# Optimization experiments

Measured on AMD Instinct MI355X. Metric: run time of the kernel, lower is better.

Reference implementation:

```python
import jax, jax.numpy as jnp
import numpy as np

NEG_SLOPE = 0.2  # PyG GATConv default negative_slope


def setup_inputs() -> dict:
    key = jax.random.key(0)
    k1, k2, k3, k4, k5, k6 = jax.random.split(key, 6)
    N, E, DIN, DOUT = 100000, 1600000, 128, 64
    x = jax.random.normal(k1, (N, DIN), dtype=jnp.float32)
    edge_index = jax.random.randint(k2, (2, E), 0, N, dtype=jnp.int64)
    # learned params (glorot-like scale)
    W = jax.random.normal(k3, (DIN, DOUT), dtype=jnp.float32) * (1.0 / np.sqrt(DIN))
    att_src = jax.random.normal(k4, (DOUT,), dtype=jnp.float32) * (1.0 / np.sqrt(DOUT))
    att_dst = jax.random.normal(k5, (DOUT,), dtype=jnp.float32) * (1.0 / np.sqrt(DOUT))
    bias = jnp.zeros((DOUT,), dtype=jnp.float32)
    return {"x": x, "edge_index": edge_index, "W": W,
            "att_src": att_src, "att_dst": att_dst, "bias": bias}


def reference(x, edge_index, W, att_src, att_dst, bias):
    N = x.shape[0]
    # add self loops (PyG default add_self_loops=True)
    loop = jnp.arange(N, dtype=edge_index.dtype)
    src = jnp.concatenate([edge_index[0], loop])  # message sources (x_j)
    dst = jnp.concatenate([edge_index[1], loop])  # aggregation targets (x_i)

    h = x @ W                         # [N, C] linear transform (heads=1)
    a_src = h @ att_src               # [N] per-node source score
    a_dst = h @ att_dst               # [N] per-node target score

    # per-edge raw attention: LeakyReLU(alpha_j + alpha_i)
    e = jax.nn.leaky_relu(a_src[src] + a_dst[dst], NEG_SLOPE)  # [Etot]

    # segment softmax over edges grouped by destination node
    e_max = jax.ops.segment_max(e, dst, num_segments=N)        # every node has self loop
    e_exp = jnp.exp(e - e_max[dst])
    e_sum = jax.ops.segment_sum(e_exp, dst, num_segments=N)
    alpha = e_exp / (e_sum[dst] + 1e-16)                       # [Etot]

    # weighted scatter-add aggregation
    out = jax.ops.segment_sum(h[src] * alpha[:, None], dst, num_segments=N)
    return out + bias
```

## Files before the change

### kernel.cpp

```cpp
#include <hip/hip_runtime.h>
#include <cstddef>

#define DIN 128
#define DOUT 64
#define BKT_SHIFT 7
#define BKT_NODES 128
#define CAP 2680
#define CAPP 2816
#define MAXB 800
#define EPB 8192
#define TW 784

#define QDEC (0.25f / 32767.f)
#define QENC (32767.f / 0.25f)

typedef __attribute__((ext_vector_type(8))) short bf16x8;
typedef __attribute__((ext_vector_type(4))) float f32x4;

__device__ __forceinline__ float leakyrelu(float v) { return v > 0.f ? v : 0.2f * v; }

__device__ __forceinline__ unsigned cvtpk(float lo, float hi) {
    unsigned r;
    asm volatile("v_cvt_pk_bf16_f32 %0, %1, %2" : "=v"(r) : "v"(lo), "v"(hi));
    return r;
}
__device__ __forceinline__ bf16x8 cvt8(f32x4 lo, f32x4 hi) {
    union { bf16x8 v; unsigned u[4]; } cv;
    cv.u[0] = cvtpk(lo[0], lo[1]);
    cv.u[1] = cvtpk(lo[2], lo[3]);
    cv.u[2] = cvtpk(hi[0], hi[1]);
    cv.u[3] = cvtpk(hi[2], hi[3]);
    return cv.v;
}

template<int T>
__device__ __forceinline__ int block_incl_scan(int v, int tid, volatile int* wscr) {
    int s = v;
    #pragma unroll
    for (int d = 1; d < 64; d <<= 1) {
        int t = __shfl_up(s, d);
        if ((tid & 63) >= d) s += t;
    }
    if ((tid & 63) == 63) wscr[tid >> 6] = s;
    __syncthreads();
    constexpr int NW = T / 64;
    if (tid < NW) {
        int w = wscr[tid];
        int sw = w;
        #pragma unroll
        for (int d = 1; d < NW; d <<= 1) {
            int t = __shfl_up(sw, d);
            if (tid >= d) sw += t;
        }
        wscr[tid] = sw - w;
    }
    __syncthreads();
    return s + wscr[tid >> 6];
}

__global__ __launch_bounds__(1024) void k_front(
    const float* __restrict__ x, const float* __restrict__ W,
    const float* __restrict__ att_src, const float* __restrict__ att_dst,
    signed char* __restrict__ h8, float2* __restrict__ sa2, float* __restrict__ adst,
    const int* __restrict__ src, const int* __restrict__ dst,
    unsigned int* __restrict__ sorted, int* __restrict__ table,
    int N, int E, int NB, int NBT)
{
    __shared__ unsigned int sbufL[EPB];
    __shared__ int hist[MAXB];
    __shared__ int offA[MAXB + 1];
    __shared__ int wscr[16];
    const int tid = threadIdx.x;

    if (blockIdx.x < NBT) {
        unsigned short* wlds = (unsigned short*)sbufL;
        {
            const int col = tid & 63;
            const int kg  = tid >> 6;
            float v[8];
            #pragma unroll
            for (int i = 0; i < 8; ++i) v[i] = W[(size_t)(kg * 8 + i) * DOUT + col];
            unsigned p0 = cvtpk(v[0], v[1]);
            unsigned p1 = cvtpk(v[2], v[3]);
            unsigned p2 = cvtpk(v[4], v[5]);
            unsigned p3 = cvtpk(v[6], v[7]);
            const int kbyte = (kg * 16) ^ ((col & 15) << 4);
            *reinterpret_cast<uint4*>((char*)wlds + col * 256 + kbyte) =
                make_uint4(p0, p1, p2, p3);
        }
        __syncthreads();

        const int lane = tid & 63, g = lane >> 4, c15 = lane & 15;
        const int n0w = blockIdx.x * 512 + (tid >> 6) * 32;
        if (n0w >= N) return;

        bf16x8 afrag[2][4];
        #pragma unroll
        for (int u = 0; u < 2; ++u) {
            const int arow = min(n0w + u * 16 + c15, N - 1);
            const float* xr = x + (size_t)arow * DIN + g * 8;
            #pragma unroll
            for (int kb = 0; kb < 4; ++kb) {
                f32x4 lo = *reinterpret_cast<const f32x4*>(xr + kb * 32);
                f32x4 hi = *reinterpret_cast<const f32x4*>(xr + kb * 32 + 4);
                afrag[u][kb] = cvt8(lo, hi);
            }
        }

        f32x4 acc[2][4];
        #pragma unroll
        for (int nt = 0; nt < 4; ++nt) {
            f32x4 a0 = {0.f, 0.f, 0.f, 0.f};
            f32x4 a1 = {0.f, 0.f, 0.f, 0.f};
            const int col = nt * 16 + c15;
            #pragma unroll
            for (int kb = 0; kb < 4; ++kb) {
                const int kbyte = (kb * 64 + g * 16) ^ (c15 << 4);
                bf16x8 bfr = *reinterpret_cast<const bf16x8*>(
                    (const char*)wlds + col * 256 + kbyte);
                a0 = __builtin_amdgcn_mfma_f32_16x16x32_bf16(afrag[0][kb], bfr, a0, 0, 0, 0);
                a1 = __builtin_amdgcn_mfma_f32_16x16x32_bf16(afrag[1][kb], bfr, a1, 0, 0, 0);
            }
            acc[0][nt] = a0;
            acc[1][nt] = a1;
        }

        #pragma unroll
        for (int u = 0; u < 2; ++u) {
            float mr[4];
            #pragma unroll
            for (int r = 0; r < 4; ++r) {
                float m = fabsf(acc[u][0][r]);
                #pragma unroll
                for (int nt = 1; nt < 4; ++nt) m = fmaxf(m, fabsf(acc[u][nt][r]));
                mr[r] = m;
            }
            #pragma unroll
            for (int mask = 1; mask < 16; mask <<= 1)
                #pragma unroll
                for (int r = 0; r < 4; ++r) mr[r] = fmaxf(mr[r], __shfl_xor(mr[r], mask));

            float inv[4];
            #pragma unroll
            for (int r = 0; r < 4; ++r) inv[r] = 127.f / fmaxf(mr[r], 1e-20f);

            #pragma unroll
            for (int nt = 0; nt < 4; ++nt)
                #pragma unroll
                for (int r = 0; r < 4; ++r) {
                    int row = n0w + u * 16 + g * 4 + r;
                    if (row < N) {
                        int qi = __float2int_rn(acc[u][nt][r] * inv[r]);
                        qi = max(-127, min(127, qi));
                        h8[(size_t)row * DOUT + nt * 16 + c15] = (signed char)qi;
                    }
                }

            float ps[4] = {0.f, 0.f, 0.f, 0.f}, pd[4] = {0.f, 0.f, 0.f, 0.f};
            #pragma unroll
            for (int nt = 0; nt < 4; ++nt) {
                float as = att_src[nt * 16 + c15];
                float ad = att_dst[nt * 16 + c15];
                #pragma unroll
                for (int r = 0; r < 4; ++r) {
                    ps[r] = fmaf(acc[u][nt][r], as, ps[r]);
                    pd[r] = fmaf(acc[u][nt][r], ad, pd[r]);
                }
            }
            #pragma unroll
            for (int mask = 1; mask < 16; mask <<= 1)
                #pragma unroll
                for (int r = 0; r < 4; ++r) {
                    ps[r] += __shfl_xor(ps[r], mask);
                    pd[r] += __shfl_xor(pd[r], mask);
                }
            #pragma unroll
            for (int r = 0; r < 4; ++r) {
                int row = n0w + u * 16 + g * 4 + r;
                if (c15 == r && row < N) {
                    sa2[row] = make_float2(ps[r], fmaxf(mr[r], 1e-20f) * (1.f / 127.f));
                    adst[row] = pd[r];
                }
            }
        }
        return;
    }

    const int c = blockIdx.x - NBT;
    const int e0 = c * EPB;
    const int cnt = min(EPB, E - e0);

    for (int i = tid; i < NB; i += 1024) hist[i] = 0;
    __syncthreads();

    unsigned pv[8]; int bv[8], rv[8];
    #pragma unroll
    for (int k = 0; k < 8; ++k) {
        int e = e0 + k * 1024 + tid;
        if (e < E) {
            int d = dst[e];
            pv[k] = (unsigned)src[e] | ((unsigned)(d & (BKT_NODES - 1)) << 17);
            bv[k] = d >> BKT_SHIFT;
            rv[k] = atomicAdd(&hist[bv[k]], 1);
        } else bv[k] = -1;
    }
    __syncthreads();

    {
        int v = (tid < NB) ? hist[tid] : 0;
        int incl = block_incl_scan<1024>(v, tid, wscr);
        if (tid < NB) offA[tid + 1] = incl;
        if (tid == 0) offA[0] = 0;
    }
    __syncthreads();

    for (int i = tid; i <= NB; i += 1024) table[(size_t)c * TW + i] = offA[i];

    #pragma unroll
    for (int k = 0; k < 8; ++k)
        if (bv[k] >= 0) sbufL[offA[bv[k]] + rv[k]] = pv[k];
    __syncthreads();

    for (int i = tid; i < cnt; i += 1024)
        sorted[(size_t)c * EPB + i] = sbufL[i];
}

__global__ __launch_bounds__(512) void k_csr(
    const unsigned int* __restrict__ sorted, const int* __restrict__ table,
    const float2* __restrict__ sa2, const float* __restrict__ adst,
    unsigned int* __restrict__ cpk, int2* __restrict__ nspan,
    int N, int NC)
{
    __shared__ unsigned int el[CAP];
    __shared__ float eal[CAP];
    __shared__ unsigned char rnk[CAP];
    __shared__ int cpre[513];
    __shared__ int cs0[512];
    __shared__ int hist[BKT_NODES], offs[BKT_NODES + 1];
    __shared__ float ssumL[BKT_NODES], selfC[BKT_NODES], adL[BKT_NODES];
    __shared__ int wscr[8];

    const int tid = threadIdx.x;
    const int b = blockIdx.x;
    const int n0 = b << BKT_SHIFT;
    const int nn = min(BKT_NODES, N - n0);

    int len = 0;
    if (tid < NC) {
        int s0 = table[(size_t)tid * TW + b];
        len = table[(size_t)tid * TW + b + 1] - s0;
        cs0[tid] = s0;
    }
    {
        int incl = block_incl_scan<512>((tid < NC) ? len : 0, tid, wscr);
        if (tid < NC) cpre[tid + 1] = incl;
        if (tid == 0) cpre[0] = 0;
    }
    if (tid < BKT_NODES) hist[tid] = 0;
    if (tid < nn) {
        int n = n0 + tid;
        float ad = adst[n];
        adL[tid] = ad;
        float2 v = sa2[n];
        float selfA = __expf(leakyrelu(v.x + ad));
        ssumL[tid] = selfA;
        selfC[tid] = selfA * v.y;
    }
    __syncthreads();
    int cnt = cpre[NC]; if (cnt > CAP) cnt = CAP;

    for (int i = tid; i < cnt; i += 512) {
        int lo = 0, hi = NC;
        while (hi - lo > 1) {
            int mid = (lo + hi) >> 1;
            if (cpre[mid] <= i) lo = mid; else hi = mid;
        }
        el[i] = sorted[(size_t)lo * EPB + cs0[lo] + (i - cpre[lo])];
    }
    __syncthreads();

    for (int i = tid; i < cnt; i += 512) {
        unsigned int e = el[i];
        int ln = e >> 17;
        float2 vs = sa2[e & 0x1FFFF];
        float a = __expf(leakyrelu(vs.x + adL[ln]));
        eal[i] = a * vs.y;
        rnk[i] = (unsigned char)atomicAdd(&hist[ln], 1);
        atomicAdd(&ssumL[ln], a);
    }
    __syncthreads();
    if (tid < nn) ssumL[tid] = 1.f / (ssumL[tid] + 1e-16f);

    {
        int v = (tid < BKT_NODES) ? hist[tid] + 1 : 0;
        int incl = block_incl_scan<512>(v, tid, wscr);
        if (tid < BKT_NODES) offs[tid + 1] = incl;
        if (tid == 0) offs[0] = 0;
    }
    __syncthreads();

    const size_t gbase = (size_t)b * CAPP;
    for (int i = tid; i < cnt; i += 512) {
        unsigned int e = el[i];
        int ln = e >> 17;
        unsigned int s = e & 0x1FFFF;
        int p = offs[ln] + (int)rnk[i];
        float cq = eal[i] * ssumL[ln];
        unsigned q = (unsigned)fminf(cq * QENC + 0.5f, 32767.f);
        cpk[gbase + p] = s | (q << 17);
    }
    __syncthreads();

    if (tid < nn) {
        int n = n0 + tid;
        int pend = offs[tid + 1];
        float cq = selfC[tid] * ssumL[tid];
        unsigned q = (unsigned)fminf(cq * QENC + 0.5f, 32767.f);
        cpk[gbase + pend - 1] = (unsigned)n | (q << 17);
        nspan[n] = make_int2((int)gbase + offs[tid], (int)gbase + pend);
    }
}

__global__ __launch_bounds__(256) void k_agg(
    const int2* __restrict__ nspan, const unsigned int* __restrict__ cpk,
    const signed char* __restrict__ h8, const float* __restrict__ bias,
    float* __restrict__ out, int N)
{
    const int lane = threadIdx.x & 63;
    const int c15 = lane & 15;
    const int grp = lane >> 4;
    const int n = blockIdx.x * 4 + (threadIdx.x >> 6);
    if (n >= N) return;
    const int2 span = nspan[n];
    const int st = span.x, en = span.y;

    const float4 bv = *reinterpret_cast<const float4*>(bias + c15 * 4);

    int acc0 = 0, acc1 = 0, acc2 = 0, acc3 = 0;
    for (int base = st; base < en; base += 32) {
        unsigned mdl = cpk[min(base + (lane & 31), en - 1)];
        unsigned mdq[8]; int qv[8]; unsigned hw[8];
        #pragma unroll
        for (int t = 0; t < 8; ++t) mdq[t] = __shfl(mdl, t * 4 + grp);
        #pragma unroll
        for (int t = 0; t < 8; ++t) {
            int e = base + t * 4 + grp;
            qv[t] = (e < en) ? (int)(mdq[t] >> 17) : 0;
        }
        #pragma unroll
        for (int t = 0; t < 8; ++t)
            hw[t] = *reinterpret_cast<const unsigned*>(
                h8 + (size_t)(mdq[t] & 0x1FFFFu) * DOUT + c15 * 4);
        #pragma unroll
        for (int t = 0; t < 8; ++t) {
            acc0 += __mul24(qv[t], (int)(signed char)(hw[t]));
            acc1 += __mul24(qv[t], (int)(signed char)(hw[t] >> 8));
            acc2 += __mul24(qv[t], (int)(signed char)(hw[t] >> 16));
            acc3 += __mul24(qv[t], (int)(signed char)(hw[t] >> 24));
        }
    }

    acc0 += __shfl_xor(acc0, 16); acc0 += __shfl_xor(acc0, 32);
    acc1 += __shfl_xor(acc1, 16); acc1 += __shfl_xor(acc1, 32);
    acc2 += __shfl_xor(acc2, 16); acc2 += __shfl_xor(acc2, 32);
    acc3 += __shfl_xor(acc3, 16); acc3 += __shfl_xor(acc3, 32);

    if (grp == 0) {
        float4 r;
        r.x = (float)acc0 * QDEC + bv.x;
        r.y = (float)acc1 * QDEC + bv.y;
        r.z = (float)acc2 * QDEC + bv.z;
        r.w = (float)acc3 * QDEC + bv.w;
        *reinterpret_cast<float4*>(out + (size_t)n * DOUT + c15 * 4) = r;
    }
}

extern "C" void kernel_launch(void* const* d_in, const int* in_sizes, int n_in,
                              void* d_out, int out_size, void* d_ws, size_t ws_size,
                              hipStream_t stream)
{
    const float* x       = (const float*)d_in[0];
    const int*   edge    = (const int*)d_in[1];
    const float* W       = (const float*)d_in[2];
    const float* att_src = (const float*)d_in[3];
    const float* att_dst = (const float*)d_in[4];
    const float* bias    = (const float*)d_in[5];

    const int N = in_sizes[0] / DIN;
    const int E = in_sizes[1] / 2;
    const int* src = edge;
    const int* dst = edge + E;
    float* out = (float*)d_out;

    const int NB = (N + BKT_NODES - 1) >> BKT_SHIFT;
    const int NC = (E + EPB - 1) / EPB;
    const int NBT = (N + 511) / 512;

    signed char* h8 = (signed char*)d_ws;
    float2* sa2 = (float2*)(h8 + (size_t)N * DOUT);
    float* adst = (float*)(sa2 + N);
    int2* nspan = (int2*)(adst + N);
    unsigned int* sorted = (unsigned int*)(nspan + N);
    int* table = (int*)(sorted + (size_t)NC * EPB);
    unsigned int* cpk = (unsigned int*)(table + (size_t)NC * TW);

    k_front<<<NBT + NC, 1024, 0, stream>>>(x, W, att_src, att_dst, h8, sa2, adst,
                                           src, dst, sorted, table, N, E, NB, NBT);
    k_csr  <<<NB, 512, 0, stream>>>(sorted, table, sa2, adst, cpk, nspan, N, NC);
    k_agg  <<<(N + 3) / 4, 256, 0, stream>>>(nspan, cpk, h8, bias, out, N);
}
```

Measured before the change: 81.61 us.

## Fuse CSR build and aggregation into one kernel using LDS-resident edge list

Merges the CSR-construction kernel and the aggregation kernel. Each 128-node bucket now keeps its packed (src, coefficient) edge list in shared memory and aggregates directly from there, which removes the global cpk/nspan round trip and one launch. The h8 quantized write is also changed to pack four bytes per row into a single 32-bit store, with the channel layout permuted so each lane owns 4 adjacent bytes, and the aggregation output is un-permuted to match. In exchange, the fused kernel runs only NB blocks (about 782) of 512 threads with more LDS per block. That may reduce parallelism and latency hiding for the gather-heavy aggregation compared with the previous 25000-block launch.

```diff
diff --git a/kernel.cpp b/kernel.cpp
--- a/kernel.cpp
+++ b/kernel.cpp
@@ -145,16 +145,19 @@
             for (int r = 0; r < 4; ++r) inv[r] = 127.f / fmaxf(mr[r], 1e-20f);
 
             #pragma unroll
-            for (int nt = 0; nt < 4; ++nt)
-                #pragma unroll
-                for (int r = 0; r < 4; ++r) {
-                    int row = n0w + u * 16 + g * 4 + r;
-                    if (row < N) {
+            for (int r = 0; r < 4; ++r) {
+                int row = n0w + u * 16 + g * 4 + r;
+                if (row < N) {
+                    unsigned pw = 0;
+                    #pragma unroll
+                    for (int nt = 0; nt < 4; ++nt) {
                         int qi = __float2int_rn(acc[u][nt][r] * inv[r]);
                         qi = max(-127, min(127, qi));
-                        h8[(size_t)row * DOUT + nt * 16 + c15] = (signed char)qi;
+                        pw |= ((unsigned)(qi & 0xFF)) << (8 * nt);
                     }
+                    *reinterpret_cast<unsigned*>(h8 + (size_t)row * DOUT + c15 * 4) = pw;
                 }
+            }
 
             float ps[4] = {0.f, 0.f, 0.f, 0.f}, pd[4] = {0.f, 0.f, 0.f, 0.f};
             #pragma unroll
@@ -225,15 +228,16 @@
         sorted[(size_t)c * EPB + i] = sbufL[i];
 }
 
-__global__ __launch_bounds__(512) void k_csr(
+__global__ __launch_bounds__(512) void k_fused(
     const unsigned int* __restrict__ sorted, const int* __restrict__ table,
     const float2* __restrict__ sa2, const float* __restrict__ adst,
-    unsigned int* __restrict__ cpk, int2* __restrict__ nspan,
-    int N, int NC)
+    const signed char* __restrict__ h8, const float* __restrict__ bias,
+    float* __restrict__ out, int N, int NC)
 {
     __shared__ unsigned int el[CAP];
     __shared__ float eal[CAP];
     __shared__ unsigned char rnk[CAP];
+    __shared__ unsigned int cpkL[CAPP];
     __shared__ int cpre[513];
     __shared__ int cs0[512];
     __shared__ int hist[BKT_NODES], offs[BKT_NODES + 1];
@@ -299,7 +303,6 @@
     }
     __syncthreads();
 
-    const size_t gbase = (size_t)b * CAPP;
     for (int i = tid; i < cnt; i += 512) {
         unsigned int e = el[i];
         int ln = e >> 17;
@@ -307,71 +310,60 @@
         int p = offs[ln] + (int)rnk[i];
         float cq = eal[i] * ssumL[ln];
         unsigned q = (unsigned)fminf(cq * QENC + 0.5f, 32767.f);
-        cpk[gbase + p] = s | (q << 17);
-    }
-    __syncthreads();
-
+        cpkL[p] = s | (q << 17);
+    }
     if (tid < nn) {
-        int n = n0 + tid;
         int pend = offs[tid + 1];
         float cq = selfC[tid] * ssumL[tid];
         unsigned q = (unsigned)fminf(cq * QENC + 0.5f, 32767.f);
-        cpk[gbase + pend - 1] = (unsigned)n | (q << 17);
-        nspan[n] = make_int2((int)gbase + offs[tid], (int)gbase + pend);
-    }
-}
-
-__global__ __launch_bounds__(256) void k_agg(
-    const int2* __restrict__ nspan, const unsigned int* __restrict__ cpk,
-    const signed char* __restrict__ h8, const float* __restrict__ bias,
-    float* __restrict__ out, int N)
-{
-    const int lane = threadIdx.x & 63;
+        cpkL[pend - 1] = (unsigned)(n0 + tid) | (q << 17);
+    }
+    __syncthreads();
+
+    const int lane = tid & 63;
     const int c15 = lane & 15;
     const int grp = lane >> 4;
-    const int n = blockIdx.x * 4 + (threadIdx.x >> 6);
-    if (n >= N) return;
-    const int2 span = nspan[n];
-    const int st = span.x, en = span.y;
-
-    const float4 bv = *reinterpret_cast<const float4*>(bias + c15 * 4);
-
-    int acc0 = 0, acc1 = 0, acc2 = 0, acc3 = 0;
-    for (int base = st; base < en; base += 32) {
-        unsigned mdl = cpk[min(base + (lane & 31), en - 1)];
-        unsigned mdq[8]; int qv[8]; unsigned hw[8];
-        #pragma unroll
-        for (int t = 0; t < 8; ++t) mdq[t] = __shfl(mdl, t * 4 + grp);
-        #pragma unroll
-        for (int t = 0; t < 8; ++t) {
-            int e = base + t * 4 + grp;
-            qv[t] = (e < en) ? (int)(mdq[t] >> 17) : 0;
-        }
-        #pragma unroll
-        for (int t = 0; t < 8; ++t)
-            hw[t] = *reinterpret_cast<const unsigned*>(
-                h8 + (size_t)(mdq[t] & 0x1FFFFu) * DOUT + c15 * 4);
-        #pragma unroll
-        for (int t = 0; t < 8; ++t) {
-            acc0 += __mul24(qv[t], (int)(signed char)(hw[t]));
-            acc1 += __mul24(qv[t], (int)(signed char)(hw[t] >> 8));
-            acc2 += __mul24(qv[t], (int)(signed char)(hw[t] >> 16));
-            acc3 += __mul24(qv[t], (int)(signed char)(hw[t] >> 24));
-        }
-    }
-
-    acc0 += __shfl_xor(acc0, 16); acc0 += __shfl_xor(acc0, 32);
-    acc1 += __shfl_xor(acc1, 16); acc1 += __shfl_xor(acc1, 32);
-    acc2 += __shfl_xor(acc2, 16); acc2 += __shfl_xor(acc2, 32);
-    acc3 += __shfl_xor(acc3, 16); acc3 += __shfl_xor(acc3, 32);
-
-    if (grp == 0) {
-        float4 r;
-        r.x = (float)acc0 * QDEC + bv.x;
-        r.y = (float)acc1 * QDEC + bv.y;
-        r.z = (float)acc2 * QDEC + bv.z;
-        r.w = (float)acc3 * QDEC + bv.w;
-        *reinterpret_cast<float4*>(out + (size_t)n * DOUT + c15 * 4) = r;
+    const int w = tid >> 6;
+    float bv[4];
+    #pragma unroll
+    for (int j = 0; j < 4; ++j) bv[j] = bias[j * 16 + c15];
+
+    for (int ln = w; ln < nn; ln += 8) {
+        const int st = offs[ln], en = offs[ln + 1];
+        int a0 = 0, a1 = 0, a2 = 0, a3 = 0;
+        for (int base = st; base < en; base += 32) {
+            unsigned mdl = cpkL[min(base + (lane & 31), en - 1)];
+            unsigned mdq[8]; int qv[8]; unsigned hw[8];
+            #pragma unroll
+            for (int t = 0; t < 8; ++t) mdq[t] = __shfl(mdl, t * 4 + grp);
+            #pragma unroll
+            for (int t = 0; t < 8; ++t) {
+                int e = base + t * 4 + grp;
+                qv[t] = (e < en) ? (int)(mdq[t] >> 17) : 0;
+            }
+            #pragma unroll
+            for (int t = 0; t < 8; ++t)
+                hw[t] = *reinterpret_cast<const unsigned*>(
+                    h8 + (size_t)(mdq[t] & 0x1FFFFu) * DOUT + c15 * 4);
+            #pragma unroll
+            for (int t = 0; t < 8; ++t) {
+                a0 += __mul24(qv[t], (int)(signed char)(hw[t]));
+                a1 += __mul24(qv[t], (int)(signed char)(hw[t] >> 8));
+                a2 += __mul24(qv[t], (int)(signed char)(hw[t] >> 16));
+                a3 += __mul24(qv[t], (int)(signed char)(hw[t] >> 24));
+            }
+        }
+        a0 += __shfl_xor(a0, 16); a0 += __shfl_xor(a0, 32);
+        a1 += __shfl_xor(a1, 16); a1 += __shfl_xor(a1, 32);
+        a2 += __shfl_xor(a2, 16); a2 += __shfl_xor(a2, 32);
+        a3 += __shfl_xor(a3, 16); a3 += __shfl_xor(a3, 32);
+        if (grp == 0) {
+            const size_t ob = (size_t)(n0 + ln) * DOUT + c15;
+            out[ob]      = (float)a0 * QDEC + bv[0];
+            out[ob + 16] = (float)a1 * QDEC + bv[1];
+            out[ob + 32] = (float)a2 * QDEC + bv[2];
+            out[ob + 48] = (float)a3 * QDEC + bv[3];
+        }
     }
 }
 
@@ -399,13 +391,10 @@
     signed char* h8 = (signed char*)d_ws;
     float2* sa2 = (float2*)(h8 + (size_t)N * DOUT);
     float* adst = (float*)(sa2 + N);
-    int2* nspan = (int2*)(adst + N);
-    unsigned int* sorted = (unsigned int*)(nspan + N);
+    unsigned int* sorted = (unsigned int*)(adst + N);
     int* table = (int*)(sorted + (size_t)NC * EPB);
-    unsigned int* cpk = (unsigned int*)(table + (size_t)NC * TW);
 
     k_front<<<NBT + NC, 1024, 0, stream>>>(x, W, att_src, att_dst, h8, sa2, adst,
                                            src, dst, sorted, table, N, E, NB, NBT);
-    k_csr  <<<NB, 512, 0, stream>>>(sorted, table, sa2, adst, cpk, nspan, N, NC);
-    k_agg  <<<(N + 3) / 4, 256, 0, stream>>>(nspan, cpk, h8, bias, out, N);
-}
+    k_fused<<<NB, 512, 0, stream>>>(sorted, table, sa2, adst, h8, bias, out, N, NC);
+}
```

Measured after the change: 84.19 us. 3.1% more time.
